# Kernel tuning notes

Hardware: AMD Instinct MI355X
Metric: run time of the kernel (lower is better)

The kernel has to match this reference:

```python
import jax, jax.numpy as jnp
import numpy as np

B, N, DIM = 4, 2048, 1024
HEAD = 16
INTER = 1024
HD = INTER // HEAD  # 64
SCALE = INTER ** (-0.5)


def setup_inputs() -> dict:
    key = jax.random.key(0)
    k1, k2, k3 = jax.random.split(key, 3)
    features = jax.random.normal(k1, (B, N, DIM), dtype=jnp.float32)
    W_qkv = jax.random.normal(k2, (DIM, 3 * INTER), dtype=jnp.float32) * (DIM ** -0.5)
    W_out = jax.random.normal(k3, (INTER, DIM), dtype=jnp.float32) * (INTER ** -0.5)
    return {"features": features, "W_qkv": W_qkv, "W_out": W_out}


def reference(features, W_qkv, W_out):
    # fc_qkv: [b, n, 3*inter], chunk into q, k, v
    qkv = jnp.einsum('bnd,de->bne', features, W_qkv)
    q, k, v = jnp.split(qkv, 3, axis=-1)
    # b n (h d) -> b n h d
    q = q.reshape(B, N, HEAD, HD)
    k = k.reshape(B, N, HEAD, HD)
    v = v.reshape(B, N, HEAD, HD)
    # scores: b h i j  (scale = inter_dim ** -0.5, as in source)
    alpha = jnp.einsum('bihd,bjhd->bhij', q, k) * SCALE
    att = jax.nn.softmax(alpha, axis=-1)
    out = jnp.einsum('bhij,bjhd->bihd', att, v)
    out = out.reshape(B, N, INTER)
    # fc_out (dropout_ratio=0.0 -> identity)
    return jnp.einsum('bni,id->bnd', out, W_out)
```

## Files before the change

### kernel.cpp

```cpp
#include <hip/hip_runtime.h>
#include <stdint.h>

#define BB 4
#define SEQ 2048
#define DMODEL 1024
#define NHEAD 16
#define HDIM 64
#define INTER 1024
#define QSCALE 0.045084220027780106f

#if __has_builtin(__builtin_amdgcn_exp2f)
#define EXP2F(x) __builtin_amdgcn_exp2f(x)
#else
#define EXP2F(x) exp2f(x)
#endif

typedef unsigned short u16;
typedef __attribute__((ext_vector_type(4))) unsigned short u16x4;
typedef __attribute__((ext_vector_type(4))) short s16x4;
typedef __attribute__((ext_vector_type(8))) short s16x8;
typedef __attribute__((ext_vector_type(4))) float f32x4;
typedef __attribute__((ext_vector_type(16))) float f32x16;
typedef __attribute__((ext_vector_type(4))) unsigned int u32x4;

__device__ __forceinline__ u16 f2bf(float f) {
  unsigned int u = __float_as_uint(f);
  u += 0x7FFFu + ((u >> 16) & 1u);
  return (u16)(u >> 16);
}

#if __has_builtin(__builtin_amdgcn_cvt_pk_bf16_f32)
typedef __attribute__((ext_vector_type(2))) __bf16 bf16x2_t;
__device__ __forceinline__ unsigned int pk2bf(float a, float b) {
  bf16x2_t r = __builtin_amdgcn_cvt_pk_bf16_f32(a, b);
  return *reinterpret_cast<unsigned int*>(&r);
}
#else
__device__ __forceinline__ unsigned int pk2bf(float a, float b) {
  return (unsigned int)f2bf(a) | ((unsigned int)f2bf(b) << 16);
}
#endif

__device__ __forceinline__ void async16(const u16* g, u16* l) {
  __builtin_amdgcn_global_load_lds((__attribute__((address_space(1))) void*)(void*)(g),
                                   (__attribute__((address_space(3))) void*)(l),
                                   16, 0, 0);
}

__device__ __forceinline__ void make_pb(const unsigned int* cc, int half,
                                        s16x8& pb0, s16x8& pb1) {
#if __has_builtin(__builtin_amdgcn_permlane32_swap)
  (void)half;
  auto r02 = __builtin_amdgcn_permlane32_swap(cc[0], cc[2], false, false);
  auto r13 = __builtin_amdgcn_permlane32_swap(cc[1], cc[3], false, false);
  auto r46 = __builtin_amdgcn_permlane32_swap(cc[4], cc[6], false, false);
  auto r57 = __builtin_amdgcn_permlane32_swap(cc[5], cc[7], false, false);
  u32x4 w0 = {(unsigned)r02[0], (unsigned)r13[0], (unsigned)r02[1], (unsigned)r13[1]};
  u32x4 w1 = {(unsigned)r46[0], (unsigned)r57[0], (unsigned)r46[1], (unsigned)r57[1]};
#else
  unsigned x0 = __shfl_xor((int)cc[0], 32, 64), x1 = __shfl_xor((int)cc[1], 32, 64);
  unsigned x2 = __shfl_xor((int)cc[2], 32, 64), x3 = __shfl_xor((int)cc[3], 32, 64);
  unsigned x4 = __shfl_xor((int)cc[4], 32, 64), x5 = __shfl_xor((int)cc[5], 32, 64);
  unsigned x6 = __shfl_xor((int)cc[6], 32, 64), x7 = __shfl_xor((int)cc[7], 32, 64);
  u32x4 w0 = {half ? x2 : cc[0], half ? x3 : cc[1],
              half ? cc[2] : x0, half ? cc[3] : x1};
  u32x4 w1 = {half ? x6 : cc[4], half ? x7 : cc[5],
              half ? cc[6] : x4, half ? cc[7] : x5};
#endif
  pb0 = *reinterpret_cast<s16x8*>(&w0);
  pb1 = *reinterpret_cast<s16x8*>(&w1);
}

__global__ __launch_bounds__(256) void prep(
    const float* __restrict__ f, const float* __restrict__ wqkv,
    const float* __restrict__ wout, u16* __restrict__ Xb,
    u16* __restrict__ WqkvT, u16* __restrict__ WoutT) {
  __shared__ float tile[32][33];
  const int bid = blockIdx.x, tid = threadIdx.x;
  if (bid < 8192) {
    int i = (bid * 256 + tid) * 4;
    f32x4 v = *reinterpret_cast<const f32x4*>(f + i);
    uint2 o;
    o.x = pk2bf(v[0], v[1]);
    o.y = pk2bf(v[2], v[3]);
    *reinterpret_cast<uint2*>(Xb + i) = o;
  } else {
    const float* src; u16* dst; int rows, cols, bx, by;
    if (bid < 8192 + 3072) {
      int t = bid - 8192;
      src = wqkv; dst = WqkvT; rows = DMODEL; cols = 3 * INTER;
      bx = t % 96; by = t / 96;
    } else {
      int t = bid - 11264;
      src = wout; dst = WoutT; rows = INTER; cols = DMODEL;
      bx = t & 31; by = t >> 5;
    }
    int c0 = bx * 32, r0 = by * 32, tx = tid & 31, ty = tid >> 5;
    #pragma unroll
    for (int i = ty; i < 32; i += 8) tile[i][tx] = src[(size_t)(r0 + i) * cols + c0 + tx];
    __syncthreads();
    #pragma unroll
    for (int i = ty; i < 32; i += 8)
      dst[(size_t)(c0 + i) * rows + r0 + tx] = f2bf(tile[tx][i]);
  }
}

template <int MODE>
__global__ __launch_bounds__(256, 2) void gemm_bt(
    const u16* __restrict__ A, const u16* __restrict__ BT,
    float* __restrict__ Cf, u16* __restrict__ Qb, u16* __restrict__ Kp,
    u16* __restrict__ Vp, int K, int ldc) {
  __shared__ u16 As[128 * 32];
  __shared__ u16 Bs[128 * 32];
  const int tid = threadIdx.x;
  const int wave = tid >> 6, lane = tid & 63;
  const int row0 = blockIdx.y * 128, col0 = blockIdx.x * 128;
  const int wr = (wave >> 1) * 64, wc = (wave & 1) * 64;
  const int r = lane & 15, q8 = (lane >> 4) * 8;

  f32x4 acc[4][4] = {};

  const int sRow = lane >> 2, sK = (lane & 3) * 8;
  const u16* Ag0 = A + (size_t)(row0 + wave * 32 + sRow) * K + sK;
  const u16* Ag1 = Ag0 + (size_t)16 * K;
  const u16* Bg0 = BT + (size_t)(col0 + wave * 32 + sRow) * K + sK;
  const u16* Bg1 = Bg0 + (size_t)16 * K;
  u16* Al0 = &As[wave * 1024];
  u16* Al1 = Al0 + 512;
  u16* Bl0 = &Bs[wave * 1024];
  u16* Bl1 = Bl0 + 512;

  for (int k0 = 0; k0 < K; k0 += 32) {
    async16(Ag0 + k0, Al0);
    async16(Ag1 + k0, Al1);
    async16(Bg0 + k0, Bl0);
    async16(Bg1 + k0, Bl1);
    __syncthreads();
    s16x8 af[4], bf[4];
    #pragma unroll
    for (int t = 0; t < 4; t++) {
      af[t] = *reinterpret_cast<const s16x8*>(&As[(wr + t * 16 + r) * 32 + q8]);
      bf[t] = *reinterpret_cast<const s16x8*>(&Bs[(wc + t * 16 + r) * 32 + q8]);
    }
    #pragma unroll
    for (int i = 0; i < 4; i++)
      #pragma unroll
      for (int j = 0; j < 4; j++)
        acc[i][j] = __builtin_amdgcn_mfma_f32_16x16x32_bf16(af[i], bf[j], acc[i][j], 0, 0, 0);
    __syncthreads();
  }

  const int quad = lane >> 4;
  #pragma unroll
  for (int i = 0; i < 4; i++) {
    const int n = row0 + wr + i * 16 + quad * 4;
    const int b = n >> 11, nn = n & (SEQ - 1);
    #pragma unroll
    for (int j = 0; j < 4; j++) {
      const int gc = col0 + wc + j * 16 + r;
      if (MODE == 1) {
        #pragma unroll
        for (int reg = 0; reg < 4; reg++)
          Cf[(size_t)(n + reg) * ldc + gc] = acc[i][j][reg];
      } else if (gc < INTER) {
        size_t base = (size_t)n * INTER + gc;
        #pragma unroll
        for (int reg = 0; reg < 4; reg++)
          Qb[base + (size_t)reg * INTER] = f2bf(acc[i][j][reg] * QSCALE);
      } else if (gc < 2 * INTER) {
        int dim = gc - INTER, h = dim >> 6, d = dim & 63;
        int bh = b * NHEAD + h;
        size_t base = (((size_t)(bh * 64 + (nn >> 5)) * 4 + (d >> 4)) * 64 +
                       ((((d >> 3) & 1) << 5) | (nn & 31))) * 8 + (d & 7);
        #pragma unroll
        for (int reg = 0; reg < 4; reg++)
          Kp[base + reg * 8] = f2bf(acc[i][j][reg]);
      } else {
        int dim = gc - 2 * INTER, h = dim >> 6, d = dim & 63;
        int bh = b * NHEAD + h;
        size_t base = ((((size_t)(bh * 64 + (nn >> 5)) * 2 + ((nn >> 4) & 1)) * 2 +
                        (d >> 5)) * 64 +
                       ((((nn >> 3) & 1) << 5) | (d & 31))) * 8 + (nn & 7);
        uint2 pk;
        pk.x = pk2bf(acc[i][j][0], acc[i][j][1]);
        pk.y = pk2bf(acc[i][j][2], acc[i][j][3]);
        *reinterpret_cast<uint2*>(Vp + base) = pk;
      }
    }
  }
}

#define ATTN_STEP(JCUR, KC, KN)                                                   \
  {                                                                               \
    const int jnext = ((JCUR) + 1) & 63;                                          \
    _Pragma("unroll")                                                             \
    for (int c = 0; c < 4; c++)                                                   \
      KN[c] = *reinterpret_cast<const s16x8*>(kpb + jnext * 2048 + c * 512);      \
    s16x8 vf[4];                                                                  \
    _Pragma("unroll")                                                             \
    for (int c = 0; c < 4; c++)                                                   \
      vf[c] = *reinterpret_cast<const s16x8*>(vpb + (JCUR) * 2048 + c * 512);     \
    f32x16 st = {};                                                               \
    __builtin_amdgcn_s_setprio(1);                                                \
    _Pragma("unroll")                                                             \
    for (int c = 0; c < 4; c++)                                                   \
      st = __builtin_amdgcn_mfma_f32_32x32x16_bf16(KC[c], qf[c], st, 0, 0, 0);    \
    __builtin_amdgcn_s_setprio(0);                                                \
    unsigned int cc[8];                                                           \
    _Pragma("unroll")                                                             \
    for (int q = 0; q < 4; q++) {                                                 \
      float p0 = EXP2F(st[q * 4 + 0]), p1 = EXP2F(st[q * 4 + 1]);                 \
      float p2 = EXP2F(st[q * 4 + 2]), p3 = EXP2F(st[q * 4 + 3]);                 \
      ls += (p0 + p1) + (p2 + p3);                                                \
      cc[q * 2 + 0] = pk2bf(p0, p1);                                              \
      cc[q * 2 + 1] = pk2bf(p2, p3);                                              \
    }                                                                             \
    s16x8 pb0, pb1;                                                               \
    make_pb(cc, half, pb0, pb1);                                                  \
    __builtin_amdgcn_s_setprio(1);                                                \
    ot0 = __builtin_amdgcn_mfma_f32_32x32x16_bf16(vf[0], pb0, ot0, 0, 0, 0);      \
    ot1 = __builtin_amdgcn_mfma_f32_32x32x16_bf16(vf[1], pb0, ot1, 0, 0, 0);      \
    ot0 = __builtin_amdgcn_mfma_f32_32x32x16_bf16(vf[2], pb1, ot0, 0, 0, 0);      \
    ot1 = __builtin_amdgcn_mfma_f32_32x32x16_bf16(vf[3], pb1, ot1, 0, 0, 0);      \
    __builtin_amdgcn_s_setprio(0);                                                \
  }

__global__ __launch_bounds__(128, 4) void attn_kernel(
    const u16* __restrict__ Qb, const u16* __restrict__ Kp,
    const u16* __restrict__ Vp, u16* __restrict__ AO) {
  const int tid = threadIdx.x;
  const int wave = tid >> 6, lane = tid & 63;
  const int l31 = lane & 31, half = lane >> 5;
  const int wg = blockIdx.x;
  const int xcd = wg & 7, li = wg >> 3;
  const int bh = xcd + ((li >> 5) << 3);
  const int iblk = li & 31;
  const int b = bh >> 4, h = bh & 15;
  const int i0 = iblk * 64 + wave * 32;

  const u16* qbase = Qb + (size_t)(b * SEQ + i0 + l31) * INTER + h * HDIM + half * 8;
  s16x8 qf[4];
  #pragma unroll
  for (int c = 0; c < 4; c++) qf[c] = *reinterpret_cast<const s16x8*>(qbase + c * 16);

  const u16* kpb = Kp + (size_t)bh * (64 * 4 * 512) + lane * 8;
  const u16* vpb = Vp + (size_t)bh * (64 * 4 * 512) + lane * 8;

  f32x16 ot0 = {}, ot1 = {};
  float ls = 0.f;

  s16x8 kf0[4], kf1[4];
  #pragma unroll
  for (int c = 0; c < 4; c++)
    kf0[c] = *reinterpret_cast<const s16x8*>(kpb + c * 512);

  for (int jb = 0; jb < 64; jb += 2) {
    ATTN_STEP(jb, kf0, kf1)
    ATTN_STEP(jb + 1, kf1, kf0)
  }

  ls += __shfl_xor(ls, 32, 64);
  float rinv = 1.0f / ls;

  u16* orow = AO + (size_t)(b * SEQ + i0 + l31) * INTER + h * HDIM;
  #pragma unroll
  for (int dt = 0; dt < 2; dt++) {
    const f32x16& o = dt ? ot1 : ot0;
    #pragma unroll
    for (int q = 0; q < 4; q++) {
      uint2 pk;
      pk.x = pk2bf(o[q * 4 + 0] * rinv, o[q * 4 + 1] * rinv);
      pk.y = pk2bf(o[q * 4 + 2] * rinv, o[q * 4 + 3] * rinv);
      *reinterpret_cast<uint2*>(orow + dt * 32 + q * 8 + half * 4) = pk;
    }
  }
}

extern "C" void kernel_launch(void* const* d_in, const int* in_sizes, int n_in,
                              void* d_out, int out_size, void* d_ws, size_t ws_size,
                              hipStream_t stream) {
  const float* features = (const float*)d_in[0];
  const float* W_qkv    = (const float*)d_in[1];
  const float* W_out    = (const float*)d_in[2];
  float* out = (float*)d_out;
  char* w = (char*)d_ws;
  u16* Xb    = (u16*)(w);
  u16* WqkvT = (u16*)(w + 16777216);
  u16* WoutT = (u16*)(w + 23068672);
  u16* Qb    = (u16*)(w + 25165824);
  u16* Kp    = (u16*)(w + 41943040);
  u16* Vp    = (u16*)(w + 58720256);
  u16* AO    = (u16*)(w + 75497472);

  prep<<<dim3(12288), dim3(256), 0, stream>>>(features, W_qkv, W_out, Xb, WqkvT, WoutT);
  gemm_bt<0><<<dim3(24, 64), dim3(256), 0, stream>>>(Xb, WqkvT, nullptr, Qb, Kp, Vp,
                                                     DMODEL, 0);
  attn_kernel<<<dim3(64 * 32), dim3(128), 0, stream>>>(Qb, Kp, Vp, AO);
  gemm_bt<1><<<dim3(8, 64), dim3(256), 0, stream>>>(AO, WoutT, out, nullptr, nullptr,
                                                    nullptr, INTER, DMODEL);
}
```

Measured before the change: 315.7 us.

## Process two 32-row query tiles per wave in attention to reuse K/V fragments

Each attention wave now handles 64 query rows as two 32-row tiles, so every K and V fragment load feeds twice as many MFMAs. The grid shrinks to 64x16 blocks with simple bh/row indexing, which drops the XCD-aware remapping. setprio hints are removed, and launch bounds drop to 2 blocks per SM to make room for the doubled accumulators. In exchange, the higher register pressure lowers occupancy and there are half as many blocks to hide latency.

Result: faster. 283.3 us (-10.2%).

```diff
diff --git a/kernel.cpp b/kernel.cpp
--- a/kernel.cpp
+++ b/kernel.cpp
@@ -190,7 +190,7 @@
   }
 }
 
-#define ATTN_STEP(JCUR, KC, KN)                                                   \
+#define ATTN_STEP2(JCUR, KC, KN)                                                  \
   {                                                                               \
     const int jnext = ((JCUR) + 1) & 63;                                          \
     _Pragma("unroll")                                                             \
@@ -200,54 +200,61 @@
     _Pragma("unroll")                                                             \
     for (int c = 0; c < 4; c++)                                                   \
       vf[c] = *reinterpret_cast<const s16x8*>(vpb + (JCUR) * 2048 + c * 512);     \
-    f32x16 st = {};                                                               \
-    __builtin_amdgcn_s_setprio(1);                                                \
+    f32x16 stA = {}, stB = {};                                                    \
     _Pragma("unroll")                                                             \
-    for (int c = 0; c < 4; c++)                                                   \
-      st = __builtin_amdgcn_mfma_f32_32x32x16_bf16(KC[c], qf[c], st, 0, 0, 0);    \
-    __builtin_amdgcn_s_setprio(0);                                                \
-    unsigned int cc[8];                                                           \
+    for (int c = 0; c < 4; c++) {                                                 \
+      stA = __builtin_amdgcn_mfma_f32_32x32x16_bf16(KC[c], qfA[c], stA, 0, 0, 0); \
+      stB = __builtin_amdgcn_mfma_f32_32x32x16_bf16(KC[c], qfB[c], stB, 0, 0, 0); \
+    }                                                                             \
+    unsigned int ccA[8], ccB[8];                                                  \
     _Pragma("unroll")                                                             \
     for (int q = 0; q < 4; q++) {                                                 \
-      float p0 = EXP2F(st[q * 4 + 0]), p1 = EXP2F(st[q * 4 + 1]);                 \
-      float p2 = EXP2F(st[q * 4 + 2]), p3 = EXP2F(st[q * 4 + 3]);                 \
-      ls += (p0 + p1) + (p2 + p3);                                                \
-      cc[q * 2 + 0] = pk2bf(p0, p1);                                              \
-      cc[q * 2 + 1] = pk2bf(p2, p3);                                              \
+      float a0 = EXP2F(stA[q * 4 + 0]), a1 = EXP2F(stA[q * 4 + 1]);               \
+      float a2 = EXP2F(stA[q * 4 + 2]), a3 = EXP2F(stA[q * 4 + 3]);               \
+      lsA += (a0 + a1) + (a2 + a3);                                               \
+      ccA[q * 2 + 0] = pk2bf(a0, a1);                                             \
+      ccA[q * 2 + 1] = pk2bf(a2, a3);                                             \
+      float b0 = EXP2F(stB[q * 4 + 0]), b1 = EXP2F(stB[q * 4 + 1]);               \
+      float b2 = EXP2F(stB[q * 4 + 2]), b3 = EXP2F(stB[q * 4 + 3]);               \
+      lsB += (b0 + b1) + (b2 + b3);                                               \
+      ccB[q * 2 + 0] = pk2bf(b0, b1);                                             \
+      ccB[q * 2 + 1] = pk2bf(b2, b3);                                             \
     }                                                                             \
-    s16x8 pb0, pb1;                                                               \
-    make_pb(cc, half, pb0, pb1);                                                  \
-    __builtin_amdgcn_s_setprio(1);                                                \
-    ot0 = __builtin_amdgcn_mfma_f32_32x32x16_bf16(vf[0], pb0, ot0, 0, 0, 0);      \
-    ot1 = __builtin_amdgcn_mfma_f32_32x32x16_bf16(vf[1], pb0, ot1, 0, 0, 0);      \
-    ot0 = __builtin_amdgcn_mfma_f32_32x32x16_bf16(vf[2], pb1, ot0, 0, 0, 0);      \
-    ot1 = __builtin_amdgcn_mfma_f32_32x32x16_bf16(vf[3], pb1, ot1, 0, 0, 0);      \
-    __builtin_amdgcn_s_setprio(0);                                                \
-  }
-
-__global__ __launch_bounds__(128, 4) void attn_kernel(
+    s16x8 pA0, pA1, pB0, pB1;                                                     \
+    make_pb(ccA, half, pA0, pA1);                                                 \
+    make_pb(ccB, half, pB0, pB1);                                                 \
+    ot0a = __builtin_amdgcn_mfma_f32_32x32x16_bf16(vf[0], pA0, ot0a, 0, 0, 0);    \
+    ot1a = __builtin_amdgcn_mfma_f32_32x32x16_bf16(vf[1], pA0, ot1a, 0, 0, 0);    \
+    ot0b = __builtin_amdgcn_mfma_f32_32x32x16_bf16(vf[0], pB0, ot0b, 0, 0, 0);    \
+    ot1b = __builtin_amdgcn_mfma_f32_32x32x16_bf16(vf[1], pB0, ot1b, 0, 0, 0);    \
+    ot0a = __builtin_amdgcn_mfma_f32_32x32x16_bf16(vf[2], pA1, ot0a, 0, 0, 0);    \
+    ot1a = __builtin_amdgcn_mfma_f32_32x32x16_bf16(vf[3], pA1, ot1a, 0, 0, 0);    \
+    ot0b = __builtin_amdgcn_mfma_f32_32x32x16_bf16(vf[2], pB1, ot0b, 0, 0, 0);    \
+    ot1b = __builtin_amdgcn_mfma_f32_32x32x16_bf16(vf[3], pB1, ot1b, 0, 0, 0);    \
+  }
+
+__global__ __launch_bounds__(128, 2) void attn_kernel(
     const u16* __restrict__ Qb, const u16* __restrict__ Kp,
     const u16* __restrict__ Vp, u16* __restrict__ AO) {
   const int tid = threadIdx.x;
   const int wave = tid >> 6, lane = tid & 63;
   const int l31 = lane & 31, half = lane >> 5;
-  const int wg = blockIdx.x;
-  const int xcd = wg & 7, li = wg >> 3;
-  const int bh = xcd + ((li >> 5) << 3);
-  const int iblk = li & 31;
-  const int b = bh >> 4, h = bh & 15;
-  const int i0 = iblk * 64 + wave * 32;
+  const int bh = blockIdx.x, b = bh >> 4, h = bh & 15;
+  const int i0 = blockIdx.y * 128 + wave * 64;
 
   const u16* qbase = Qb + (size_t)(b * SEQ + i0 + l31) * INTER + h * HDIM + half * 8;
-  s16x8 qf[4];
+  s16x8 qfA[4], qfB[4];
   #pragma unroll
-  for (int c = 0; c < 4; c++) qf[c] = *reinterpret_cast<const s16x8*>(qbase + c * 16);
+  for (int c = 0; c < 4; c++) {
+    qfA[c] = *reinterpret_cast<const s16x8*>(qbase + c * 16);
+    qfB[c] = *reinterpret_cast<const s16x8*>(qbase + (size_t)32 * INTER + c * 16);
+  }
 
   const u16* kpb = Kp + (size_t)bh * (64 * 4 * 512) + lane * 8;
   const u16* vpb = Vp + (size_t)bh * (64 * 4 * 512) + lane * 8;
 
-  f32x16 ot0 = {}, ot1 = {};
-  float ls = 0.f;
+  f32x16 ot0a = {}, ot1a = {}, ot0b = {}, ot1b = {};
+  float lsA = 0.f, lsB = 0.f;
 
   s16x8 kf0[4], kf1[4];
   #pragma unroll
@@ -255,23 +262,30 @@
     kf0[c] = *reinterpret_cast<const s16x8*>(kpb + c * 512);
 
   for (int jb = 0; jb < 64; jb += 2) {
-    ATTN_STEP(jb, kf0, kf1)
-    ATTN_STEP(jb + 1, kf1, kf0)
-  }
-
-  ls += __shfl_xor(ls, 32, 64);
-  float rinv = 1.0f / ls;
-
-  u16* orow = AO + (size_t)(b * SEQ + i0 + l31) * INTER + h * HDIM;
+    ATTN_STEP2(jb, kf0, kf1)
+    ATTN_STEP2(jb + 1, kf1, kf0)
+  }
+
+  lsA += __shfl_xor(lsA, 32, 64);
+  lsB += __shfl_xor(lsB, 32, 64);
+  float rinvA = 1.0f / lsA;
+  float rinvB = 1.0f / lsB;
+
+  u16* orowA = AO + (size_t)(b * SEQ + i0 + l31) * INTER + h * HDIM;
+  u16* orowB = orowA + (size_t)32 * INTER;
   #pragma unroll
   for (int dt = 0; dt < 2; dt++) {
-    const f32x16& o = dt ? ot1 : ot0;
+    const f32x16& oa = dt ? ot1a : ot0a;
+    const f32x16& ob = dt ? ot1b : ot0b;
     #pragma unroll
     for (int q = 0; q < 4; q++) {
-      uint2 pk;
-      pk.x = pk2bf(o[q * 4 + 0] * rinv, o[q * 4 + 1] * rinv);
-      pk.y = pk2bf(o[q * 4 + 2] * rinv, o[q * 4 + 3] * rinv);
-      *reinterpret_cast<uint2*>(orow + dt * 32 + q * 8 + half * 4) = pk;
+      uint2 pka, pkb;
+      pka.x = pk2bf(oa[q * 4 + 0] * rinvA, oa[q * 4 + 1] * rinvA);
+      pka.y = pk2bf(oa[q * 4 + 2] * rinvA, oa[q * 4 + 3] * rinvA);
+      *reinterpret_cast<uint2*>(orowA + dt * 32 + q * 8 + half * 4) = pka;
+      pkb.x = pk2bf(ob[q * 4 + 0] * rinvB, ob[q * 4 + 1] * rinvB);
+      pkb.y = pk2bf(ob[q * 4 + 2] * rinvB, ob[q * 4 + 3] * rinvB);
+      *reinterpret_cast<uint2*>(orowB + dt * 32 + q * 8 + half * 4) = pkb;
     }
   }
 }
@@ -295,7 +309,7 @@
   prep<<<dim3(12288), dim3(256), 0, stream>>>(features, W_qkv, W_out, Xb, WqkvT, WoutT);
   gemm_bt<0><<<dim3(24, 64), dim3(256), 0, stream>>>(Xb, WqkvT, nullptr, Qb, Kp, Vp,
                                                      DMODEL, 0);
-  attn_kernel<<<dim3(64 * 32), dim3(128), 0, stream>>>(Qb, Kp, Vp, AO);
+  attn_kernel<<<dim3(64, 16), dim3(128), 0, stream>>>(Qb, Kp, Vp, AO);
   gemm_bt<1><<<dim3(8, 64), dim3(256), 0, stream>>>(AO, WoutT, out, nullptr, nullptr,
                                                     nullptr, INTER, DMODEL);
 }
```
